# Kernel optimization log

Measured on AMD Instinct MI355X. Metric: run time of the kernel, lower is better.

The kernel has to match this reference:

```python
import jax, jax.numpy as jnp
import numpy as np

# ---- dopri5 (RK45) tableau ----
C2, C3, C4, C5 = 1/5, 3/10, 4/5, 8/9
A21 = 1/5
A31, A32 = 3/40, 9/40
A41, A42, A43 = 44/45, -56/15, 32/9
A51, A52, A53, A54 = 19372/6561, -25360/2187, 64448/6561, -212/729
A61, A62, A63, A64, A65 = 9017/3168, -355/33, 46732/5247, 49/176, -5103/18656
B1, B3, B4, B5, B6 = 35/384, 500/1113, 125/192, -2187/6784, 11/84
# error coefficients = b(5th) - b(4th)
E1, E3, E4, E5, E6, E7 = 71/57600, -71/16695, 71/1920, -17253/339200, 22/525, -1/40

N_STEPS = 24          # fixed scan length for the adaptive loop (jit-friendly)
RTOL = ATOL = 1e-3    # tolerance from init_kwargs
DT0 = 0.1             # initial step size


def conv_time(t, x, w, b, padding):
    # append time as an extra channel, then NCHW conv
    t_img = jnp.full_like(x[:, :1], t)
    xt = jnp.concatenate([t_img, x], axis=1)
    y = jax.lax.conv_general_dilated(xt, w, (1, 1), padding,
                                     dimension_numbers=('NCHW', 'OIHW', 'NCHW'))
    return y + b[None, :, None, None]


def ode_func(t, x, w1, b1, w2, b2, w3, b3):
    h = jax.nn.relu(conv_time(t, x, w1, b1, [(0, 0), (0, 0)]))
    h = jax.nn.relu(conv_time(t, h, w2, b2, [(1, 1), (1, 1)]))
    return conv_time(t, h, w3, b3, [(0, 0), (0, 0)])


def dopri5_step(f, t, y, dt):
    k1 = f(t, y)
    k2 = f(t + dt * C2, y + dt * (A21 * k1))
    k3 = f(t + dt * C3, y + dt * (A31 * k1 + A32 * k2))
    k4 = f(t + dt * C4, y + dt * (A41 * k1 + A42 * k2 + A43 * k3))
    k5 = f(t + dt * C5, y + dt * (A51 * k1 + A52 * k2 + A53 * k3 + A54 * k4))
    k6 = f(t + dt, y + dt * (A61 * k1 + A62 * k2 + A63 * k3 + A64 * k4 + A65 * k5))
    y5 = y + dt * (B1 * k1 + B3 * k3 + B4 * k4 + B5 * k5 + B6 * k6)
    k7 = f(t + dt, y5)  # FSAL stage, used for error estimate
    err = dt * (E1 * k1 + E3 * k3 + E4 * k4 + E5 * k5 + E6 * k6 + E7 * k7)
    return y5, err


def integrate(f, y0):
    """Adaptive dopri5 from t=0 to t=1 with fixed-length masked scan."""
    def step(carry, _):
        t, y, dt = carry
        dt_c = jnp.minimum(dt, 1.0 - t)
        y_new, err = dopri5_step(f, t, y, dt_c)
        tol = ATOL + RTOL * jnp.maximum(jnp.abs(y), jnp.abs(y_new))
        err_norm = jnp.sqrt(jnp.mean((err / tol) ** 2))
        done = t >= 1.0 - 1e-7
        adv = (err_norm <= 1.0) & (~done)
        t_n = jnp.where(adv, t + dt_c, t)
        y_n = jnp.where(adv, y_new, y)
        safe = jnp.maximum(err_norm, 1e-10)
        factor = jnp.clip(0.9 * safe ** (-0.2), 0.2, 10.0)
        dt_n = jnp.where(done, dt, dt_c * factor)
        return (t_n, y_n, dt_n), None

    step = jax.checkpoint(step)
    (t, y, dt), _ = jax.lax.scan(step,
                                 (jnp.float32(0.0), y0, jnp.float32(DT0)),
                                 None, length=N_STEPS)
    return y


def setup_inputs() -> dict:
    key = jax.random.key(0)
    ks = jax.random.split(key, 9)
    B, Cin, H, W = 64, 3, 32, 32
    AUG, NF = 5, 64
    CH = Cin + AUG  # 8
    x = jax.random.normal(ks[0], (B, Cin, H, W), dtype=jnp.float32)
    def wgt(k, shape):
        fan_in = shape[1] * shape[2] * shape[3]
        return jax.random.normal(k, shape, dtype=jnp.float32) / np.sqrt(fan_in).astype(np.float32)
    w1 = wgt(ks[1], (NF, CH + 1, 1, 1)); b1 = jnp.zeros((NF,), jnp.float32)
    w2 = wgt(ks[2], (NF, NF + 1, 3, 3)); b2 = jnp.zeros((NF,), jnp.float32)
    w3 = wgt(ks[3], (CH, NF + 1, 1, 1)); b3 = jnp.zeros((CH,), jnp.float32)
    flat = CH * H * W  # 8192
    wl = jax.random.normal(ks[4], (10, flat), dtype=jnp.float32) / np.sqrt(flat).astype(np.float32)
    bl = jnp.zeros((10,), jnp.float32)
    return {"x": x, "w1": w1, "b1": b1, "w2": w2, "b2": b2,
            "w3": w3, "b3": b3, "wl": wl, "bl": bl}


def reference(x, w1, b1, w2, b2, w3, b3, wl, bl):
    B, C, H, W = x.shape
    AUG = w3.shape[0] - C  # augmented channels
    aug = jnp.zeros((B, AUG, H, W), dtype=x.dtype)
    y0 = jnp.concatenate([x, aug], axis=1)
    f = lambda t, y: ode_func(t, y, w1, b1, w2, b2, w3, b3)
    yT = integrate(f, y0)                    # state at t = 1
    out = yT.reshape(B, -1) @ wl.T + bl      # final linear head
    return out
```

## Files before the change

### kernel.cpp

```cpp
#include <hip/hip_runtime.h>
#include <math.h>

namespace {
constexpr int BN = 64;
constexpr int HW = 1024;
constexpr int NS = BN*8*HW;

constexpr float C2f = 0.2f, C3f = 0.3f, C4f = 0.8f, C5f = (float)(8.0/9.0);
constexpr float A21 = 0.2f;
constexpr float A31 = (float)(3.0/40.0),  A32 = (float)(9.0/40.0);
constexpr float A41 = (float)(44.0/45.0), A42 = (float)(-56.0/15.0), A43 = (float)(32.0/9.0);
constexpr float A51 = (float)(19372.0/6561.0), A52 = (float)(-25360.0/2187.0),
                A53 = (float)(64448.0/6561.0), A54 = (float)(-212.0/729.0);
constexpr float A61 = (float)(9017.0/3168.0), A62 = (float)(-355.0/33.0),
                A63 = (float)(46732.0/5247.0), A64 = (float)(49.0/176.0),
                A65 = (float)(-5103.0/18656.0);
constexpr float B1c = (float)(35.0/384.0), B3c = (float)(500.0/1113.0),
                B4c = (float)(125.0/192.0), B5c = (float)(-2187.0/6784.0),
                B6c = (float)(11.0/84.0);
constexpr float E1c = (float)(71.0/57600.0), E3c = (float)(-71.0/16695.0),
                E4c = (float)(71.0/1920.0), E5c = (float)(-17253.0/339200.0),
                E6c = (float)(22.0/525.0),  E7c = (float)(-1.0/40.0);
constexpr float RTOL = 1e-3f, ATOL = 1e-3f;

constexpr size_t OFF_PART = 0;
constexpr size_t OFF_FLAG = 1024;
constexpr size_t OFF_CNT  = 1536;
constexpr size_t OFF_TSUM = 1600;
constexpr size_t OFF_W2P  = 2176;
constexpr size_t OFF_Y    = 20608;
constexpr size_t OFF_Y5   = OFF_Y  + (size_t)NS;
constexpr size_t OFF_K    = OFF_Y5 + (size_t)NS;
constexpr size_t OFF_WPK  = OFF_K + (size_t)7*NS;

constexpr int ACT_STRIDE = 264;
constexpr int H2_STRIDE  = 136;
}

__constant__ float g_cf[6][5] = {
    {A21, 0, 0, 0, 0},
    {A31, A32, 0, 0, 0},
    {A41, A42, A43, 0, 0},
    {A51, A52, A53, A54, 0},
    {A61, A62, A63, A64, A65},
    {0, 0, 0, 0, 0}};
__constant__ float g_ct[6] = {C2f, C3f, C4f, C5f, 1.0f, 1.0f};

typedef _Float16 hfrag8 __attribute__((ext_vector_type(8)));
typedef float f32x16 __attribute__((ext_vector_type(16)));

union HU { hfrag8 h; unsigned u[4]; };

__device__ __forceinline__ float ld_sysf(const float* p) {
    return __hip_atomic_load(p, __ATOMIC_RELAXED, __HIP_MEMORY_SCOPE_SYSTEM);
}
__device__ __forceinline__ float2 ld_sysf2(const float* p) {
    union { unsigned long long u; float2 f; } c;
    c.u = __hip_atomic_load((const unsigned long long*)p, __ATOMIC_RELAXED,
                            __HIP_MEMORY_SCOPE_SYSTEM);
    return c.f;
}
__device__ __forceinline__ void st_sysf(float* p, float v) {
    __hip_atomic_store(p, v, __ATOMIC_RELAXED, __HIP_MEMORY_SCOPE_SYSTEM);
}
__device__ __forceinline__ void st_sysf2(float* p, float a, float b) {
    union { unsigned long long u; float2 f; } c;
    c.f = make_float2(a, b);
    __hip_atomic_store((unsigned long long*)p, c.u, __ATOMIC_RELAXED,
                       __HIP_MEMORY_SCOPE_SYSTEM);
}

__device__ __forceinline__ void ld8(const float* p, float* v, bool sys) {
    if (sys) {
        #pragma unroll
        for (int h = 0; h < 4; h++) {
            float2 t = ld_sysf2(p + 2*h);
            v[2*h] = t.x; v[2*h+1] = t.y;
        }
    } else {
        float4 a = *(const float4*)p;
        float4 b = *(const float4*)(p + 4);
        v[0]=a.x; v[1]=a.y; v[2]=a.z; v[3]=a.w;
        v[4]=b.x; v[5]=b.y; v[6]=b.z; v[7]=b.w;
    }
}
__device__ __forceinline__ void st8(float* p, const float* v, bool sys) {
    if (sys) {
        st_sysf2(p,     v[0], v[1]);
        st_sysf2(p + 2, v[2], v[3]);
        st_sysf2(p + 4, v[4], v[5]);
        st_sysf2(p + 6, v[6], v[7]);
    } else {
        *(float4*)p       = make_float4(v[0], v[1], v[2], v[3]);
        *(float4*)(p + 4) = make_float4(v[4], v[5], v[6], v[7]);
    }
}

__global__ __launch_bounds__(256)
void k_init(const float* __restrict__ x, float* __restrict__ y,
            int* __restrict__ flags, unsigned* __restrict__ cnt)
{
    int idx = blockIdx.x*256 + threadIdx.x;
    int b = idx >> 13, px = (idx >> 3) & 1023, c = idx & 7;
    y[idx] = (c < 3) ? x[(size_t)(b*3 + c)*1024 + px] : 0.0f;
    if (idx < 512) flags[idx] = 0;
    if (idx == 600) *cnt = 0u;
}

__global__ __launch_bounds__(256)
void k_prepack(const float* __restrict__ w1, const float* __restrict__ w2,
               const float* __restrict__ w3, _Float16* __restrict__ w2p,
               float* __restrict__ tsum, float* __restrict__ wpk)
{
    int gid = blockIdx.x*256 + threadIdx.x;
    if (gid < 36864) {
        int j    = gid & 7;
        int lane = (gid >> 3) & 63;
        int nt   = (gid >> 9) & 1;
        int ks   = (gid >> 10) & 3;
        int tap  = gid >> 12;
        int oc = nt*32 + (lane & 31);
        int ic = ks*16 + (lane >> 5)*8 + j;
        w2p[gid] = (_Float16)w2[oc*585 + (1 + ic)*9 + tap];
    }
    if (gid < 576) {
        int oc = gid & 63, combo = gid >> 6;
        int rcase = combo / 3, ccase = combo % 3;
        float s = 0.0f;
        for (int kh = 0; kh < 3; kh++) {
            if ((rcase == 1 && kh == 0) || (rcase == 2 && kh == 2)) continue;
            for (int kw = 0; kw < 3; kw++) {
                if ((ccase == 1 && kw == 0) || (ccase == 2 && kw == 2)) continue;
                s += w2[oc*585 + kh*3 + kw];
            }
        }
        tsum[gid] = s;
    }
    if (gid < 512) wpk[gid] = w1[(gid & 63)*9 + 1 + (gid >> 6)];
    if (gid < 64)  wpk[512 + gid] = w1[gid*9];
    if (gid < 512) wpk[576 + gid] = w3[(gid & 7)*65 + 1 + (gid >> 3)];
    if (gid < 8)   wpk[1088 + gid] = w3[gid*65];
}

__global__ void __launch_bounds__(256, 2)
k_ode(const float* __restrict__ b1, const float* __restrict__ b2,
      const float* __restrict__ b3, const _Float16* __restrict__ w2p,
      const float* __restrict__ tsumg, const float* __restrict__ wpk,
      const float* __restrict__ wl, const float* __restrict__ bl,
      float* __restrict__ ybuf, float* __restrict__ y5buf,
      float* __restrict__ kb, float* __restrict__ part,
      int* __restrict__ flags, float* __restrict__ out)
{
    __shared__ __align__(16) unsigned char s_pool[53600];
    __shared__ __align__(16) unsigned char s_h2[17408];
    __shared__ __align__(16) _Float16 s_z[1552];
    __shared__ float s_tsum[576];
    __shared__ float s_b2v[64], s_b1v[64], s_w10v[64];
    __shared__ float s_w30v[8], s_b3v[8];
    __shared__ float s_red[256];

    const int tid = threadIdx.x;
    const int nblk = gridDim.x;
    const int lane = tid & 63;
    const int m32 = lane & 31, q2 = lane >> 5;
    const int rp = tid >> 7;
    const int np = (tid >> 6) & 1;
    const int wid = tid >> 6;
    const bool lz32 = (lane == 32);
    const bool lz31 = (lane == 31);

    if (tid < 64) {
        s_b2v[tid] = b2[tid];
        s_b1v[tid] = b1[tid];
        s_w10v[tid] = wpk[512 + tid];
    }
    if (tid < 8) { s_w30v[tid] = wpk[1088 + tid]; s_b3v[tid] = b3[tid]; }
    for (int i = tid; i < 576; i += 256) s_tsum[i] = tsumg[i];
    if (tid < 8) s_z[192*8 + tid] = (_Float16)0.0f;
    __syncthreads();

    const int oct1 = wid >> 1;
    hfrag8 w1f;
    #pragma unroll
    for (int j = 0; j < 8; j++)
        w1f[j] = q2 ? (_Float16)0.0f : (_Float16)wpk[j*64 + oct1*32 + m32];
    hfrag8 w3f[4];
    #pragma unroll
    for (int kst = 0; kst < 4; kst++)
        #pragma unroll
        for (int j = 0; j < 8; j++) {
            int ch = kst*16 + q2*8 + j;
            w3f[kst][j] = (m32 < 8) ? (_Float16)wpk[576 + ch*8 + m32]
                                    : (_Float16)0.0f;
        }

    float t = 0.0f, dt = 0.1f;
    float* ya = ybuf; float* yb = y5buf;
    float* ka = kb;  float* kg = kb + 6*(size_t)NS;

    auto wait_all = [&](int target) {
        for (;;) {
            bool ok = (__hip_atomic_load(&flags[tid], __ATOMIC_RELAXED,
                           __HIP_MEMORY_SCOPE_SYSTEM) >= target)
                   && (__hip_atomic_load(&flags[tid + 256], __ATOMIC_RELAXED,
                           __HIP_MEMORY_SCOPE_SYSTEM) >= target);
            if (__syncthreads_and((int)ok)) break;
            __builtin_amdgcn_s_sleep(2);
        }
    };

    auto eval = [&](const float* src, int nc, const float* cf, float ctv,
                    float* kout, int mode, int gev, float* partp) {
        float dtc = fminf(dt, 1.0f - t);
        float ts  = t + ctv*dtc;

        for (int tile = blockIdx.x; tile < 512; tile += nblk) {
            int b = tile >> 3, rg = tile & 7;

            if (tid < 192) {
                int w = tid >> 5;
                int lr = (0x504132 >> (4*w)) & 7;
                int col = tid & 31;
                int r = rg*4 - 1 + lr;
                bool sysrow = (lr < 2) | (lr > 3);
                if (gev > 1 && w >= 4) {
                    const int* fp = (lr == 0) ? &flags[tile-1] : &flags[tile+1];
                    bool need = (lr == 0) ? (rg > 0) : (rg < 7);
                    while (need && __hip_atomic_load(fp, __ATOMIC_RELAXED,
                                                     __HIP_MEMORY_SCOPE_SYSTEM) < gev-1)
                        __builtin_amdgcn_s_sleep(1);
                }
                union { _Float16 h[8]; uint4 u; } pz;
                if ((unsigned)r < 32u) {
                    int px = (r << 5) + col;
                    size_t pb8 = ((size_t)(b << 10) + px) << 3;
                    float kv[5][8], sv[8];
                    if (sysrow) {
                        #pragma unroll
                        for (int j = 0; j < 5; j++) if (j < nc) {
                            const float* kp = (j == 0 ? ka : kb + (size_t)j*NS) + pb8;
                            #pragma unroll
                            for (int h = 0; h < 4; h++) {
                                float2 t2 = ld_sysf2(kp + 2*h);
                                kv[j][2*h] = t2.x; kv[j][2*h+1] = t2.y;
                            }
                        }
                        #pragma unroll
                        for (int h = 0; h < 4; h++) {
                            float2 t2 = ld_sysf2(src + pb8 + 2*h);
                            sv[2*h] = t2.x; sv[2*h+1] = t2.y;
                        }
                    } else {
                        #pragma unroll
                        for (int j = 0; j < 5; j++) if (j < nc) {
                            const float* kp = (j == 0 ? ka : kb + (size_t)j*NS) + pb8;
                            float4 a4 = *(const float4*)kp;
                            float4 b4 = *(const float4*)(kp + 4);
                            kv[j][0]=a4.x; kv[j][1]=a4.y; kv[j][2]=a4.z; kv[j][3]=a4.w;
                            kv[j][4]=b4.x; kv[j][5]=b4.y; kv[j][6]=b4.z; kv[j][7]=b4.w;
                        }
                        float4 a4 = *(const float4*)(src + pb8);
                        float4 b4 = *(const float4*)(src + pb8 + 4);
                        sv[0]=a4.x; sv[1]=a4.y; sv[2]=a4.z; sv[3]=a4.w;
                        sv[4]=b4.x; sv[5]=b4.y; sv[6]=b4.z; sv[7]=b4.w;
                    }
                    float s[8] = {0,0,0,0,0,0,0,0};
                    #pragma unroll
                    for (int j = 0; j < 5; j++) if (j < nc) {
                        float a = cf[j];
                        #pragma unroll
                        for (int c = 0; c < 8; c++) s[c] = fmaf(a, kv[j][c], s[c]);
                    }
                    #pragma unroll
                    for (int c = 0; c < 8; c++)
                        pz.h[c] = (_Float16)(sv[c] + dtc*s[c]);
                } else {
                    pz.u = make_uint4(0u,0u,0u,0u);
                }
                *(uint4*)(s_z + (size_t)(lr*32 + col)*8) = pz.u;
            }
            __syncthreads();

            {
                int pgbase = (wid & 1)*3;
                #pragma unroll
                for (int i = 0; i < 3; i++) {
                    int pxg = pgbase + i;
                    int r = rg*4 - 1 + pxg;
                    bool valid = ((unsigned)r < 32u);
                    const _Float16* zp = s_z + (q2 ? (size_t)192*8
                                                   : (size_t)(pxg*32 + m32)*8);
                    hfrag8 bz = *(const hfrag8*)zp;
                    f32x16 a1 = (f32x16)(0.0f);
                    a1 = __builtin_amdgcn_mfma_f32_32x32x16_f16(w1f, bz, a1, 0,0,0);
                    unsigned words[8];
                    #pragma unroll
                    for (int pr = 0; pr < 8; pr++) {
                        int r0 = 2*pr;
                        int oc0 = oct1*32 + (r0&3) + 8*(r0>>2) + 4*q2;
                        float v0 = valid ? fmaxf(a1[r0]   + ts*s_w10v[oc0]
                                                 + s_b1v[oc0],   0.0f) : 0.0f;
                        float v1 = valid ? fmaxf(a1[r0+1] + ts*s_w10v[oc0+1]
                                                 + s_b1v[oc0+1], 0.0f) : 0.0f;
                        union { _Float16 h[2]; unsigned u; } pk;
                        pk.h[0] = (_Float16)v0; pk.h[1] = (_Float16)v1;
                        words[pr] = pk.u;
                    }
                    unsigned char* basep = s_pool
                        + (size_t)(pxg*34 + m32 + 1)*ACT_STRIDE + oct1*64 + q2*8;
                    #pragma unroll
                    for (int wq = 0; wq < 4; wq++)
                        *(uint2*)(basep + wq*16) =
                            make_uint2(words[2*wq], words[2*wq+1]);
                }
            }
            __syncthreads();

            f32x16 acc2[2];
            acc2[0] = (f32x16)(0.0f);
            acc2[1] = (f32x16)(0.0f);
            {
                const unsigned char* actb = (const unsigned char*)s_pool;
                #pragma unroll 1
                for (int ks = 0; ks < 4; ks++) {
                    HU fc[4], d0[4], d2[4];
                    #pragma unroll
                    for (int l = 0; l < 4; l++) {
                        const unsigned char* p = actb
                            + (size_t)((rp*2 + l)*34 + m32 + 1)*ACT_STRIDE
                            + ks*32 + q2*16;
                        *(uint2*)&fc[l].u[0] = *(const uint2*)p;
                        *(uint2*)&fc[l].u[2] = *(const uint2*)(p + 8);
                    }
                    #pragma unroll
                    for (int l = 0; l < 4; l++) {
                        #pragma unroll
                        for (int i = 0; i < 4; i++) {
                            unsigned s0 = (unsigned)__builtin_amdgcn_update_dpp(
                                0, (int)fc[l].u[i], 0x138, 0xF, 0xF, true);
                            d0[l].u[i] = lz32 ? 0u : s0;
                            unsigned s2 = (unsigned)__builtin_amdgcn_update_dpp(
                                0, (int)fc[l].u[i], 0x130, 0xF, 0xF, true);
                            d2[l].u[i] = lz31 ? 0u : s2;
                        }
                    }
                    #pragma unroll
                    for (int kh = 0; kh < 3; kh++) {
                        #pragma unroll
                        for (int kw = 0; kw < 3; kw++) {
                            int tap = kh*3 + kw;
                            hfrag8 aw = *(const hfrag8*)
                                (w2p + (size_t)((tap*4 + ks)*2 + np)*512 + lane*8);
                            #pragma unroll
                            for (int ri = 0; ri < 2; ri++) {
                                int l = ri + kh;
                                hfrag8 bf = (kw == 0) ? d0[l].h
                                          : ((kw == 1) ? fc[l].h : d2[l].h);
                                acc2[ri] = __builtin_amdgcn_mfma_f32_32x32x16_f16(
                                    aw, bf, acc2[ri], 0, 0, 0);
                            }
                        }
                    }
                }
            }

            {
                int ccase = (m32 == 0) ? 1 : ((m32 == 31) ? 2 : 0);
                #pragma unroll
                for (int ri = 0; ri < 2; ri++) {
                    int pg = rp*2 + ri;
                    int r_out = rg*4 + pg;
                    int rcase = (r_out == 0) ? 1 : ((r_out == 31) ? 2 : 0);
                    const float* tsb = &s_tsum[(rcase*3 + ccase)*64];
                    int px = pg*32 + m32;
                    unsigned words[8];
                    #pragma unroll
                    for (int pr = 0; pr < 8; pr++) {
                        int r0 = 2*pr;
                        int oc0 = np*32 + (r0&3) + 8*(r0>>2) + 4*q2;
                        float v0 = fmaxf(acc2[ri][r0]   + ts*tsb[oc0]
                                         + s_b2v[oc0],   0.0f);
                        float v1 = fmaxf(acc2[ri][r0+1] + ts*tsb[oc0+1]
                                         + s_b2v[oc0+1], 0.0f);
                        union { _Float16 h[2]; unsigned u; } pk;
                        pk.h[0] = (_Float16)v0; pk.h[1] = (_Float16)v1;
                        words[pr] = pk.u;
                    }
                    unsigned char* basep = s_h2 + (size_t)px*H2_STRIDE
                                           + np*64 + q2*8;
                    #pragma unroll
                    for (int wq = 0; wq < 4; wq++)
                        *(uint2*)(basep + wq*16) =
                            make_uint2(words[2*wq], words[2*wq+1]);
                }
            }
            __syncthreads();

            {
                f32x16 a3a = (f32x16)(0.0f);
                const unsigned char* hb = (const unsigned char*)s_h2;
                #pragma unroll
                for (int kst = 0; kst < 4; kst++) {
                    HU f;
                    const unsigned char* p = hb
                        + (size_t)(wid*32 + m32)*H2_STRIDE + kst*32 + q2*16;
                    *(uint2*)&f.u[0] = *(const uint2*)p;
                    *(uint2*)&f.u[2] = *(const uint2*)(p + 8);
                    a3a = __builtin_amdgcn_mfma_f32_32x32x16_f16(
                        w3f[kst], f.h, a3a, 0, 0, 0);
                }
                float a3[8];
                #pragma unroll
                for (int r = 0; r < 4; r++) {
                    float own = a3a[r];
                    float oth = __shfl(own, lane ^ 32, 64);
                    a3[r]     = q2 ? oth : own;
                    a3[4 + r] = q2 ? own : oth;
                }
                float ls = 0.0f;
                if (q2 == 0) {
                    #pragma unroll
                    for (int c = 0; c < 8; c++)
                        a3[c] += fmaf(ts, s_w30v[c], s_b3v[c]);
                    bool sysrow = (wid == 0) | (wid == 3);
                    int px = rg*128 + wid*32 + m32;
                    size_t pb8 = ((size_t)(b << 10) + px) << 3;
                    st8(kout + pb8, a3, sysrow);
                    if (mode == 1) {
                        float kv1[8], kv3[8], kv4[8], kv5[8], yv[8], r8[8];
                        ld8(ka + pb8, kv1, sysrow);
                        ld8(kb + 2*(size_t)NS + pb8, kv3, sysrow);
                        ld8(kb + 3*(size_t)NS + pb8, kv4, sysrow);
                        ld8(kb + 4*(size_t)NS + pb8, kv5, sysrow);
                        ld8(ya + pb8, yv, sysrow);
                        #pragma unroll
                        for (int c = 0; c < 8; c++)
                            r8[c] = yv[c] + dtc*(B1c*kv1[c] + B3c*kv3[c]
                                    + B4c*kv4[c] + B5c*kv5[c] + B6c*a3[c]);
                        st8(yb + pb8, r8, sysrow);
                    } else if (mode == 2) {
                        float kv1[8], kv3[8], kv4[8], kv5[8], kv6[8], yv[8], y5v[8];
                        ld8(ka + pb8, kv1, sysrow);
                        ld8(kb + 2*(size_t)NS + pb8, kv3, sysrow);
                        ld8(kb + 3*(size_t)NS + pb8, kv4, sysrow);
                        ld8(kb + 4*(size_t)NS + pb8, kv5, sysrow);
                        ld8(kb + 5*(size_t)NS + pb8, kv6, sysrow);
                        ld8(ya + pb8, yv, sysrow);
                        ld8(yb + pb8, y5v, sysrow);
                        #pragma unroll
                        for (int c = 0; c < 8; c++) {
                            float e = dtc*(E1c*kv1[c] + E3c*kv3[c] + E4c*kv4[c]
                                           + E5c*kv5[c] + E6c*kv6[c] + E7c*a3[c]);
                            float tol = ATOL + RTOL*fmaxf(fabsf(yv[c]), fabsf(y5v[c]));
                            float rr = e / tol;
                            ls += rr*rr;
                        }
                    }
                }
                if (mode == 2) {
                    s_red[tid] = ls;
                    __syncthreads();
                    for (int sft = 128; sft > 0; sft >>= 1) {
                        if (tid < sft) s_red[tid] += s_red[tid + sft];
                        __syncthreads();
                    }
                    if (tid == 0) st_sysf(&partp[tile], s_red[0]);
                }
            }
            __syncthreads();
            if (tid == 0)
                __hip_atomic_store(&flags[tile], gev, __ATOMIC_RELAXED,
                                   __HIP_MEMORY_SCOPE_SYSTEM);
        }
    };

    int gev = 1;
    eval(ya, 0, g_cf[5], 0.0f, ka, 0, gev, part);
    gev++;

    for (int st = 0; st < 24; st++) {
        if (t >= 1.0f - 1e-7f) break;
        float* partp = part + (size_t)(st & 1)*512;
        for (int e = 0; e < 6; e++) {
            int nc = (e < 5) ? e + 1 : 0;
            const float* src = (e == 5) ? yb : ya;
            float* kout = (e < 5) ? kb + (size_t)(e + 1)*NS : kg;
            int mode = (e == 4) ? 1 : ((e == 5) ? 2 : 0);
            eval(src, nc, g_cf[e], g_ct[e], kout, mode, gev, partp);
            gev++;
        }
        wait_all(gev - 1);
        float v = ld_sysf(&partp[tid]) + ld_sysf(&partp[tid + 256]);
        s_red[tid] = v;
        __syncthreads();
        for (int sft = 128; sft > 0; sft >>= 1) {
            if (tid < sft) s_red[tid] += s_red[tid + sft];
            __syncthreads();
        }
        float red0 = s_red[0];
        __syncthreads();
        float err_norm = sqrtf(red0 / (float)NS);
        float dtc = fminf(dt, 1.0f - t);
        bool adv = (err_norm <= 1.0f);
        if (adv) {
            t = t + dtc;
            float* tmp = ya; ya = yb; yb = tmp;
            tmp = ka; ka = kg; kg = tmp;
        }
        float safe = fmaxf(err_norm, 1e-10f);
        float factor = fminf(fmaxf(0.9f*powf(safe, -0.2f), 0.2f), 10.0f);
        dt = dtc*factor;
    }

    for (int tile = blockIdx.x; tile < 512; tile += nblk) {
        int b = tile >> 3, rg = tile & 7;
        if (tid < 128) {
            int lrow = tid >> 5;
            if (lrow == 1 || lrow == 2) {
                int px = rg*128 + tid;
                float* yp = ya + (((size_t)(b << 10) + px) << 3);
                float4 v0 = *(const float4*)yp;
                float4 v1 = *(const float4*)(yp + 4);
                st_sysf2(yp,     v0.x, v0.y);
                st_sysf2(yp + 2, v0.z, v0.w);
                st_sysf2(yp + 4, v1.x, v1.y);
                st_sysf2(yp + 6, v1.z, v1.w);
            }
        }
    }
    __syncthreads();
    for (int tile = blockIdx.x; tile < 512; tile += nblk)
        if (tid == 0)
            __hip_atomic_store(&flags[tile], gev, __ATOMIC_RELAXED,
                               __HIP_MEMORY_SCOPE_SYSTEM);
    wait_all(gev);

    for (int bh = blockIdx.x; bh < 64; bh += nblk) {
        float* s_hred = (float*)s_pool;
        float acc[10];
        #pragma unroll
        for (int m = 0; m < 10; m++) acc[m] = 0.0f;
        for (int px = tid; px < 1024; px += 256) {
            const float* yp = ya + (((size_t)(bh << 10) + px) << 3);
            float yv[8];
            #pragma unroll
            for (int h = 0; h < 4; h++) {
                float2 v = ld_sysf2(yp + 2*h);
                yv[2*h] = v.x; yv[2*h+1] = v.y;
            }
            #pragma unroll
            for (int c = 0; c < 8; c++) {
                float v = yv[c];
                #pragma unroll
                for (int m = 0; m < 10; m++)
                    acc[m] = fmaf(v, wl[(size_t)m*8192 + (c << 10) + px], acc[m]);
            }
        }
        #pragma unroll
        for (int m = 0; m < 10; m++) s_hred[m*256 + tid] = acc[m];
        __syncthreads();
        for (int sft = 128; sft > 0; sft >>= 1) {
            if (tid < sft) {
                #pragma unroll
                for (int m = 0; m < 10; m++)
                    s_hred[m*256 + tid] += s_hred[m*256 + tid + sft];
            }
            __syncthreads();
        }
        if (tid < 10) out[bh*10 + tid] = s_hred[tid*256] + bl[tid];
        __syncthreads();
    }
}

extern "C" void kernel_launch(void* const* d_in, const int* in_sizes, int n_in,
                              void* d_out, int out_size, void* d_ws, size_t ws_size,
                              hipStream_t stream)
{
    const float* x  = (const float*)d_in[0];
    const float* w1 = (const float*)d_in[1];
    const float* b1 = (const float*)d_in[2];
    const float* w2 = (const float*)d_in[3];
    const float* b2 = (const float*)d_in[4];
    const float* w3 = (const float*)d_in[5];
    const float* b3 = (const float*)d_in[6];
    const float* wl = (const float*)d_in[7];
    const float* bl = (const float*)d_in[8];
    float* out = (float*)d_out;

    float* F = (float*)d_ws;
    float* part = F + OFF_PART;
    int*   flags = (int*)(F + OFF_FLAG);
    unsigned* cnt = (unsigned*)(F + OFF_CNT);
    float* tsum = F + OFF_TSUM;
    _Float16* w2p = (_Float16*)(F + OFF_W2P);
    float* y    = F + OFF_Y;
    float* y5   = F + OFF_Y5;
    float* kbp  = F + OFF_K;
    float* wpk  = F + OFF_WPK;

    k_init<<<NS/256, 256, 0, stream>>>(x, y, flags, cnt);
    k_prepack<<<144, 256, 0, stream>>>(w1, w2, w3, w2p, tsum, wpk);

    int maxb = 0;
    if (hipOccupancyMaxActiveBlocksPerMultiprocessor(&maxb,
            reinterpret_cast<const void*>(k_ode), 256, 0) != hipSuccess || maxb < 1)
        maxb = 1;
    int cus = 256;
    {
        int dev = 0;
        hipGetDevice(&dev);
        hipDeviceProp_t prop;
        if (hipGetDeviceProperties(&prop, dev) == hipSuccess && prop.multiProcessorCount > 0)
            cus = prop.multiProcessorCount;
    }
    long cap = (long)maxb * (long)cus;
    int gridn = (int)((cap < 512) ? cap : 512);
    if (gridn < 16) gridn = 16;

    k_ode<<<gridn, 256, 0, stream>>>(b1, b2, b3, w2p, tsum, wpk, wl, bl,
                                     y, y5, kbp, part, flags, out);
}
```

Before: 464.4 us.

## Split halo flags per edge row and load stage inputs directly into MFMA fragments

Replaces the single per-tile completion flag with separate top and bottom edge-row flags, so a neighbouring tile only waits for the boundary row it needs. Those flags are published by the individual waves right after their stores drain, not after a block-wide barrier. The staging of the stage input through shared memory is removed: each wave computes its z-row fragment in registers and feeds it straight into the 1x1 conv MFMA. Channel order in the activations is permuted, with the weights repacked to match, so shared-memory reads and writes become 16-byte vector accesses. This aims to cut barrier and inter-block wait latency, but relies on finer-grained memory ordering that is subtle to get right.

```diff
diff --git a/kernel.cpp b/kernel.cpp
--- a/kernel.cpp
+++ b/kernel.cpp
@@ -32,9 +32,11 @@
 constexpr size_t OFF_Y5   = OFF_Y  + (size_t)NS;
 constexpr size_t OFF_K    = OFF_Y5 + (size_t)NS;
 constexpr size_t OFF_WPK  = OFF_K + (size_t)7*NS;
-
-constexpr int ACT_STRIDE = 264;
-constexpr int H2_STRIDE  = 136;
+constexpr size_t OFF_FT   = OFF_WPK + 1152;
+constexpr size_t OFF_FB   = OFF_FT + 512;
+
+constexpr int ACT_STRIDE = 272;
+constexpr int H2_STRIDE  = 144;
 }
 
 __constant__ float g_cf[6][5] = {
@@ -49,7 +51,7 @@
 typedef _Float16 hfrag8 __attribute__((ext_vector_type(8)));
 typedef float f32x16 __attribute__((ext_vector_type(16)));
 
-union HU { hfrag8 h; unsigned u[4]; };
+union HU { hfrag8 h; unsigned u[4]; uint4 v; };
 
 __device__ __forceinline__ float ld_sysf(const float* p) {
     return __hip_atomic_load(p, __ATOMIC_RELAXED, __HIP_MEMORY_SCOPE_SYSTEM);
@@ -98,13 +100,13 @@
 
 __global__ __launch_bounds__(256)
 void k_init(const float* __restrict__ x, float* __restrict__ y,
-            int* __restrict__ flags, unsigned* __restrict__ cnt)
+            int* __restrict__ flags, int* __restrict__ flagT,
+            int* __restrict__ flagB)
 {
     int idx = blockIdx.x*256 + threadIdx.x;
     int b = idx >> 13, px = (idx >> 3) & 1023, c = idx & 7;
     y[idx] = (c < 3) ? x[(size_t)(b*3 + c)*1024 + px] : 0.0f;
-    if (idx < 512) flags[idx] = 0;
-    if (idx == 600) *cnt = 0u;
+    if (idx < 512) { flags[idx] = 0; flagT[idx] = 0; flagB[idx] = 0; }
 }
 
 __global__ __launch_bounds__(256)
@@ -120,7 +122,9 @@
         int ks   = (gid >> 10) & 3;
         int tap  = gid >> 12;
         int oc = nt*32 + (lane & 31);
-        int ic = ks*16 + (lane >> 5)*8 + j;
+        int kpos = ks*16 + (lane >> 5)*8 + j;
+        int oct = kpos >> 5, q2b = (kpos >> 4) & 1, rr = kpos & 15;
+        int ic = oct*32 + (rr & 3) + (q2b << 2) + ((rr >> 2) << 3);
         w2p[gid] = (_Float16)w2[oc*585 + (1 + ic)*9 + tap];
     }
     if (gid < 576) {
@@ -149,11 +153,11 @@
       const float* __restrict__ wl, const float* __restrict__ bl,
       float* __restrict__ ybuf, float* __restrict__ y5buf,
       float* __restrict__ kb, float* __restrict__ part,
-      int* __restrict__ flags, float* __restrict__ out)
+      int* __restrict__ flags, int* __restrict__ flagT,
+      int* __restrict__ flagB, float* __restrict__ out)
 {
-    __shared__ __align__(16) unsigned char s_pool[53600];
-    __shared__ __align__(16) unsigned char s_h2[17408];
-    __shared__ __align__(16) _Float16 s_z[1552];
+    __shared__ __align__(16) unsigned char s_pool[192*ACT_STRIDE];
+    __shared__ __align__(16) unsigned char s_h2[128*H2_STRIDE];
     __shared__ float s_tsum[576];
     __shared__ float s_b2v[64], s_b1v[64], s_w10v[64];
     __shared__ float s_w30v[8], s_b3v[8];
@@ -176,20 +180,25 @@
     }
     if (tid < 8) { s_w30v[tid] = wpk[1088 + tid]; s_b3v[tid] = b3[tid]; }
     for (int i = tid; i < 576; i += 256) s_tsum[i] = tsumg[i];
-    if (tid < 8) s_z[192*8 + tid] = (_Float16)0.0f;
     __syncthreads();
 
-    const int oct1 = wid >> 1;
-    hfrag8 w1f;
+    hfrag8 w1lo[2], w1hi[2];
     #pragma unroll
-    for (int j = 0; j < 8; j++)
-        w1f[j] = q2 ? (_Float16)0.0f : (_Float16)wpk[j*64 + oct1*32 + m32];
+    for (int oct = 0; oct < 2; oct++)
+        #pragma unroll
+        for (int j = 0; j < 8; j++) {
+            _Float16 wv = (_Float16)wpk[j*64 + oct*32 + m32];
+            w1lo[oct][j] = q2 ? (_Float16)0.0f : wv;
+            w1hi[oct][j] = q2 ? wv : (_Float16)0.0f;
+        }
     hfrag8 w3f[4];
     #pragma unroll
     for (int kst = 0; kst < 4; kst++)
         #pragma unroll
         for (int j = 0; j < 8; j++) {
-            int ch = kst*16 + q2*8 + j;
+            int kpos = kst*16 + q2*8 + j;
+            int oct = kpos >> 5, q2b = (kpos >> 4) & 1, rr = kpos & 15;
+            int ch = oct*32 + (rr & 3) + (q2b << 2) + ((rr >> 2) << 3);
             w3f[kst][j] = (m32 < 8) ? (_Float16)wpk[576 + ch*8 + m32]
                                     : (_Float16)0.0f;
         }
@@ -217,22 +226,12 @@
         for (int tile = blockIdx.x; tile < 512; tile += nblk) {
             int b = tile >> 3, rg = tile & 7;
 
-            if (tid < 192) {
-                int w = tid >> 5;
-                int lr = (0x504132 >> (4*w)) & 7;
-                int col = tid & 31;
+            auto zload = [&](int lr) {
+                HU pz; pz.v = make_uint4(0u,0u,0u,0u);
                 int r = rg*4 - 1 + lr;
-                bool sysrow = (lr < 2) | (lr > 3);
-                if (gev > 1 && w >= 4) {
-                    const int* fp = (lr == 0) ? &flags[tile-1] : &flags[tile+1];
-                    bool need = (lr == 0) ? (rg > 0) : (rg < 7);
-                    while (need && __hip_atomic_load(fp, __ATOMIC_RELAXED,
-                                                     __HIP_MEMORY_SCOPE_SYSTEM) < gev-1)
-                        __builtin_amdgcn_s_sleep(1);
-                }
-                union { _Float16 h[8]; uint4 u; } pz;
-                if ((unsigned)r < 32u) {
-                    int px = (r << 5) + col;
+                if ((unsigned)lr < 6u && (unsigned)r < 32u) {
+                    bool sysrow = (lr < 2) | (lr > 3);
+                    int px = (r << 5) + m32;
                     size_t pb8 = ((size_t)(b << 10) + px) << 3;
                     float kv[5][8], sv[8];
                     if (sysrow) {
@@ -274,44 +273,55 @@
                     #pragma unroll
                     for (int c = 0; c < 8; c++)
                         pz.h[c] = (_Float16)(sv[c] + dtc*s[c]);
-                } else {
-                    pz.u = make_uint4(0u,0u,0u,0u);
-                }
-                *(uint4*)(s_z + (size_t)(lr*32 + col)*8) = pz.u;
-            }
-            __syncthreads();
-
+                }
+                return pz;
+            };
+
+            HU pz;
+            if (q2 == 0) pz = zload(wid + 1);
+            if (gev > 1 && q2 == 1 && (wid == 0 || wid == 3)) {
+                bool need = (wid == 0) ? (rg > 0) : (rg < 7);
+                if (need) {
+                    const int* fp = (wid == 0) ? &flagB[tile-1] : &flagT[tile+1];
+                    while (__hip_atomic_load(fp, __ATOMIC_RELAXED,
+                                             __HIP_MEMORY_SCOPE_SYSTEM) < gev-1)
+                        __builtin_amdgcn_s_sleep(1);
+                }
+            }
+            if (q2 == 1) pz = zload((wid == 0) ? 0 : ((wid == 3) ? 5 : -1));
+
+            auto wr_act = [&](int lr, const f32x16& a1, int oct, bool valid) {
+                unsigned words[8];
+                #pragma unroll
+                for (int pr = 0; pr < 8; pr++) {
+                    int r0 = 2*pr;
+                    int oc0 = oct*32 + (r0 & 3) + 8*(r0 >> 2) + 4*q2;
+                    float v0 = valid ? fmaxf(a1[r0]   + ts*s_w10v[oc0]
+                                             + s_b1v[oc0],   0.0f) : 0.0f;
+                    float v1 = valid ? fmaxf(a1[r0+1] + ts*s_w10v[oc0+1]
+                                             + s_b1v[oc0+1], 0.0f) : 0.0f;
+                    union { _Float16 h[2]; unsigned u; } pk;
+                    pk.h[0] = (_Float16)v0; pk.h[1] = (_Float16)v1;
+                    words[pr] = pk.u;
+                }
+                unsigned char* basep = s_pool + (size_t)(lr*32 + m32)*ACT_STRIDE
+                                       + oct*64 + q2*32;
+                *(uint4*)basep        = make_uint4(words[0],words[1],words[2],words[3]);
+                *(uint4*)(basep + 16) = make_uint4(words[4],words[5],words[6],words[7]);
+            };
             {
-                int pgbase = (wid & 1)*3;
-                #pragma unroll
-                for (int i = 0; i < 3; i++) {
-                    int pxg = pgbase + i;
-                    int r = rg*4 - 1 + pxg;
-                    bool valid = ((unsigned)r < 32u);
-                    const _Float16* zp = s_z + (q2 ? (size_t)192*8
-                                                   : (size_t)(pxg*32 + m32)*8);
-                    hfrag8 bz = *(const hfrag8*)zp;
-                    f32x16 a1 = (f32x16)(0.0f);
-                    a1 = __builtin_amdgcn_mfma_f32_32x32x16_f16(w1f, bz, a1, 0,0,0);
-                    unsigned words[8];
-                    #pragma unroll
-                    for (int pr = 0; pr < 8; pr++) {
-                        int r0 = 2*pr;
-                        int oc0 = oct1*32 + (r0&3) + 8*(r0>>2) + 4*q2;
-                        float v0 = valid ? fmaxf(a1[r0]   + ts*s_w10v[oc0]
-                                                 + s_b1v[oc0],   0.0f) : 0.0f;
-                        float v1 = valid ? fmaxf(a1[r0+1] + ts*s_w10v[oc0+1]
-                                                 + s_b1v[oc0+1], 0.0f) : 0.0f;
-                        union { _Float16 h[2]; unsigned u; } pk;
-                        pk.h[0] = (_Float16)v0; pk.h[1] = (_Float16)v1;
-                        words[pr] = pk.u;
-                    }
-                    unsigned char* basep = s_pool
-                        + (size_t)(pxg*34 + m32 + 1)*ACT_STRIDE + oct1*64 + q2*8;
-                    #pragma unroll
-                    for (int wq = 0; wq < 4; wq++)
-                        *(uint2*)(basep + wq*16) =
-                            make_uint2(words[2*wq], words[2*wq+1]);
+                f32x16 zz = (f32x16)(0.0f);
+                f32x16 c0 = __builtin_amdgcn_mfma_f32_32x32x16_f16(w1lo[0], pz.h, zz, 0,0,0);
+                f32x16 c1 = __builtin_amdgcn_mfma_f32_32x32x16_f16(w1lo[1], pz.h, zz, 0,0,0);
+                wr_act(wid + 1, c0, 0, true);
+                wr_act(wid + 1, c1, 1, true);
+                if (wid == 0 || wid == 3) {
+                    int lrh = (wid == 0) ? 0 : 5;
+                    bool vh = (unsigned)(rg*4 - 1 + lrh) < 32u;
+                    f32x16 d0 = __builtin_amdgcn_mfma_f32_32x32x16_f16(w1hi[0], pz.h, zz, 0,0,0);
+                    f32x16 d1 = __builtin_amdgcn_mfma_f32_32x32x16_f16(w1hi[1], pz.h, zz, 0,0,0);
+                    wr_act(lrh, d0, 0, vh);
+                    wr_act(lrh, d1, 1, vh);
                 }
             }
             __syncthreads();
@@ -327,10 +337,9 @@
                     #pragma unroll
                     for (int l = 0; l < 4; l++) {
                         const unsigned char* p = actb
-                            + (size_t)((rp*2 + l)*34 + m32 + 1)*ACT_STRIDE
+                            + (size_t)((rp*2 + l)*32 + m32)*ACT_STRIDE
                             + ks*32 + q2*16;
-                        *(uint2*)&fc[l].u[0] = *(const uint2*)p;
-                        *(uint2*)&fc[l].u[2] = *(const uint2*)(p + 8);
+                        fc[l].v = *(const uint4*)p;
                     }
                     #pragma unroll
                     for (int l = 0; l < 4; l++) {
@@ -377,7 +386,7 @@
                     #pragma unroll
                     for (int pr = 0; pr < 8; pr++) {
                         int r0 = 2*pr;
-                        int oc0 = np*32 + (r0&3) + 8*(r0>>2) + 4*q2;
+                        int oc0 = np*32 + (r0 & 3) + 8*(r0 >> 2) + 4*q2;
                         float v0 = fmaxf(acc2[ri][r0]   + ts*tsb[oc0]
                                          + s_b2v[oc0],   0.0f);
                         float v1 = fmaxf(acc2[ri][r0+1] + ts*tsb[oc0+1]
@@ -387,25 +396,22 @@
                         words[pr] = pk.u;
                     }
                     unsigned char* basep = s_h2 + (size_t)px*H2_STRIDE
-                                           + np*64 + q2*8;
-                    #pragma unroll
-                    for (int wq = 0; wq < 4; wq++)
-                        *(uint2*)(basep + wq*16) =
-                            make_uint2(words[2*wq], words[2*wq+1]);
+                                           + np*64 + q2*32;
+                    *(uint4*)basep        = make_uint4(words[0],words[1],words[2],words[3]);
+                    *(uint4*)(basep + 16) = make_uint4(words[4],words[5],words[6],words[7]);
                 }
             }
             __syncthreads();
 
+            float ls = 0.0f;
             {
                 f32x16 a3a = (f32x16)(0.0f);
-                const unsigned char* hb = (const unsigned char*)s_h2;
                 #pragma unroll
                 for (int kst = 0; kst < 4; kst++) {
                     HU f;
-                    const unsigned char* p = hb
+                    const unsigned char* p = s_h2
                         + (size_t)(wid*32 + m32)*H2_STRIDE + kst*32 + q2*16;
-                    *(uint2*)&f.u[0] = *(const uint2*)p;
-                    *(uint2*)&f.u[2] = *(const uint2*)(p + 8);
+                    f.v = *(const uint4*)p;
                     a3a = __builtin_amdgcn_mfma_f32_32x32x16_f16(
                         w3f[kst], f.h, a3a, 0, 0, 0);
                 }
@@ -417,7 +423,6 @@
                     a3[r]     = q2 ? oth : own;
                     a3[4 + r] = q2 ? own : oth;
                 }
-                float ls = 0.0f;
                 if (q2 == 0) {
                     #pragma unroll
                     for (int c = 0; c < 8; c++)
@@ -457,20 +462,27 @@
                         }
                     }
                 }
-                if (mode == 2) {
-                    s_red[tid] = ls;
+            }
+            asm volatile("s_waitcnt vmcnt(0)" ::: "memory");
+            if (lane == 0 && wid == 0)
+                __hip_atomic_store(&flagT[tile], gev, __ATOMIC_RELAXED,
+                                   __HIP_MEMORY_SCOPE_SYSTEM);
+            if (lane == 0 && wid == 3)
+                __hip_atomic_store(&flagB[tile], gev, __ATOMIC_RELAXED,
+                                   __HIP_MEMORY_SCOPE_SYSTEM);
+            if (mode == 2) {
+                s_red[tid] = ls;
+                __syncthreads();
+                for (int sft = 128; sft > 0; sft >>= 1) {
+                    if (tid < sft) s_red[tid] += s_red[tid + sft];
                     __syncthreads();
-                    for (int sft = 128; sft > 0; sft >>= 1) {
-                        if (tid < sft) s_red[tid] += s_red[tid + sft];
-                        __syncthreads();
-                    }
-                    if (tid == 0) st_sysf(&partp[tile], s_red[0]);
-                }
-            }
-            __syncthreads();
-            if (tid == 0)
-                __hip_atomic_store(&flags[tile], gev, __ATOMIC_RELAXED,
-                                   __HIP_MEMORY_SCOPE_SYSTEM);
+                }
+                if (tid == 0) st_sysf(&partp[tile], s_red[0]);
+                __syncthreads();
+                if (tid == 0)
+                    __hip_atomic_store(&flags[tile], gev, __ATOMIC_RELAXED,
+                                       __HIP_MEMORY_SCOPE_SYSTEM);
+            }
         }
     };
 
@@ -590,15 +602,16 @@
     float* F = (float*)d_ws;
     float* part = F + OFF_PART;
     int*   flags = (int*)(F + OFF_FLAG);
-    unsigned* cnt = (unsigned*)(F + OFF_CNT);
     float* tsum = F + OFF_TSUM;
     _Float16* w2p = (_Float16*)(F + OFF_W2P);
     float* y    = F + OFF_Y;
     float* y5   = F + OFF_Y5;
     float* kbp  = F + OFF_K;
     float* wpk  = F + OFF_WPK;
-
-    k_init<<<NS/256, 256, 0, stream>>>(x, y, flags, cnt);
+    int*   flagT = (int*)(F + OFF_FT);
+    int*   flagB = (int*)(F + OFF_FB);
+
+    k_init<<<NS/256, 256, 0, stream>>>(x, y, flags, flagT, flagB);
     k_prepack<<<144, 256, 0, stream>>>(w1, w2, w3, w2p, tsum, wpk);
 
     int maxb = 0;
@@ -618,5 +631,5 @@
     if (gridn < 16) gridn = 16;
 
     k_ode<<<gridn, 256, 0, stream>>>(b1, b2, b3, w2p, tsum, wpk, wl, bl,
-                                     y, y5, kbp, part, flags, out);
-}
+                                     y, y5, kbp, part, flags, flagT, flagB, out);
+}
```

After: 407.8 us. -12.2%, faster.
